# Performance work log

Measured on AMD Instinct MI355X. Metric: run time of the kernel, lower is better.

The kernel has to match this reference:

```python
import jax, jax.numpy as jnp
import numpy as np

EMBED_DIM = 1024
N_HEADS = 16

def setup_inputs() -> dict:
    key = jax.random.key(0)
    k1, k2, k3 = jax.random.split(key, 3)
    x = jax.random.normal(k1, (4, 2048, EMBED_DIM), dtype=jnp.float32)
    # nn.Linear(D, 3D): store weight as [D, 3D] for x @ W
    W_qkv = jax.random.normal(k2, (EMBED_DIM, 3 * EMBED_DIM), dtype=jnp.float32) * (1.0 / np.sqrt(EMBED_DIM))
    b_qkv = jax.random.normal(k3, (3 * EMBED_DIM,), dtype=jnp.float32) * 0.02
    return {"x": x, "W_qkv": W_qkv, "b_qkv": b_qkv}

def reference(x, W_qkv, b_qkv):
    bs, T, D = x.shape
    nh = N_HEADS
    hs = D // nh
    # fused qkv projection -> [bs, T, nh, 3, hs] (matches view(bs,T,nh,3*hs) + split(hs))
    qkv = (jnp.einsum('btd,de->bte', x, W_qkv) + b_qkv).reshape(bs, T, nh, 3, hs)
    q = qkv[..., 0, :].transpose(0, 2, 1, 3)  # [bs, nh, T, hs]
    k = qkv[..., 1, :].transpose(0, 2, 1, 3)
    v = qkv[..., 2, :].transpose(0, 2, 1, 3)
    scale = 1.0 / np.sqrt(hs).astype(np.float32)
    scores = jnp.einsum('bhqd,bhkd->bhqk', q, k) * scale  # [bs, nh, T, T]
    attn = jax.nn.softmax(scores, axis=-1)
    out = jnp.einsum('bhqk,bhkd->bhqd', attn, v)  # [bs, nh, T, hs]
    return out.transpose(0, 2, 1, 3).reshape(bs, T, D)
```

## Files before the change

kernel.cpp:

```cpp
#include <hip/hip_runtime.h>
#include <stdint.h>

#define T_SEQ 2048
#define DMODEL 1024
#define NHEAD 16
#define HS 64
#define N3 3072
#define BSZ 4
#define MTOT (BSZ*T_SEQ)

typedef __attribute__((ext_vector_type(8))) short bf16x8;
typedef __attribute__((ext_vector_type(4))) float f32x4;
typedef __attribute__((ext_vector_type(16))) float f32x16;
typedef __attribute__((ext_vector_type(2))) unsigned int uint2v;

#define QSCALE 0.18033688011112042f
#define SM_SHIFT 12.0f

#define BH_STRIDE 131072

__device__ inline unsigned short f2bf(float f){
  union { float f; uint32_t u; } v; v.f = f;
  uint32_t r = (v.u + 0x7fffu + ((v.u >> 16) & 1u)) >> 16;
  return (unsigned short)r;
}

__device__ inline uint32_t cvtpk_bf16(float lo, float hi){
  uint32_t r;
  asm("v_cvt_pk_bf16_f32 %0, %1, %2" : "=v"(r) : "v"(lo), "v"(hi));
  return r;
}

__device__ inline void plswap(uint32_t &a, uint32_t &b){
  uint2v r = __builtin_amdgcn_permlane32_swap(a, b, false, false);
  a = r[0]; b = r[1];
}

__device__ inline void gld16(const void* g, void* l){
  __builtin_amdgcn_global_load_lds((const __attribute__((address_space(1))) void*)g,
                                   (__attribute__((address_space(3))) void*)l, 16, 0, 0);
}

__global__ __launch_bounds__(256) void cvt_x(const float* __restrict__ x,
                                             unsigned short* __restrict__ xb, int n){
  int stride = gridDim.x * blockDim.x;
  for (int i = blockIdx.x * blockDim.x + threadIdx.x; i * 4 < n; i += stride){
    const float4 v = *(const float4*)(x + (size_t)i * 4);
    ushort4 o; o.x = f2bf(v.x); o.y = f2bf(v.y); o.z = f2bf(v.z); o.w = f2bf(v.w);
    *(ushort4*)(xb + (size_t)i * 4) = o;
  }
}

__global__ __launch_bounds__(256) void cvt_wt(const float* __restrict__ W,
                                              unsigned short* __restrict__ Wt){
  __shared__ float tile[32][33];
  int bx = blockIdx.x;
  int by = blockIdx.y;
  int tx = threadIdx.x;
  int ty = threadIdx.y;
#pragma unroll
  for (int i = 0; i < 4; i++){
    int k = by * 32 + ty + i * 8;
    int n = bx * 32 + tx;
    tile[ty + i * 8][tx] = W[(size_t)k * N3 + n];
  }
  __syncthreads();
#pragma unroll
  for (int i = 0; i < 4; i++){
    int n = bx * 32 + ty + i * 8;
    int k = by * 32 + tx;
    Wt[(size_t)n * DMODEL + k] = f2bf(tile[tx][ty + i * 8]);
  }
}

#define BM 128
#define BN 128
#define BK 32

__global__ __launch_bounds__(256, 2) void gemm_qkv(
    const unsigned short* __restrict__ xb, const unsigned short* __restrict__ wt,
    const float* __restrict__ bias,
    unsigned short* __restrict__ Qb, unsigned short* __restrict__ Kb,
    unsigned short* __restrict__ Vt)
{
  __shared__ unsigned short Al[2][BM * BK];
  __shared__ unsigned short Bl[2][BN * BK];
  const int tid = threadIdx.x;
  const int lane = tid & 63;
  const int w  = tid >> 6;
  const int wm = w >> 1, wn = w & 1;
  const int lr = lane & 15, lg = lane >> 4;
  const int m0 = blockIdx.x * BM;
  const int n0 = blockIdx.y * BN;

  f32x4 acc[4][4] = {};

  const int srow = tid >> 2;
  const int scol = ((tid & 3) ^ ((srow >> 1) & 3)) * 8;
  const unsigned short* ga0 = xb + (size_t)(m0 + srow) * DMODEL + scol;
  const unsigned short* gb0 = wt + (size_t)(n0 + srow) * DMODEL + scol;

  const int lgp = lg ^ ((lr >> 1) & 3);

  gld16(ga0,                         &Al[0][tid * 8]);
  gld16(ga0 + (size_t)64 * DMODEL,   &Al[0][tid * 8 + 2048]);
  gld16(gb0,                         &Bl[0][tid * 8]);
  gld16(gb0 + (size_t)64 * DMODEL,   &Bl[0][tid * 8 + 2048]);
  __syncthreads();

  for (int k0 = 0; k0 < DMODEL; k0 += BK){
    const int cur = (k0 >> 5) & 1;
    if (k0 + BK < DMODEL){
      gld16(ga0 + k0 + BK,                       &Al[cur ^ 1][tid * 8]);
      gld16(ga0 + k0 + BK + (size_t)64 * DMODEL, &Al[cur ^ 1][tid * 8 + 2048]);
      gld16(gb0 + k0 + BK,                       &Bl[cur ^ 1][tid * 8]);
      gld16(gb0 + k0 + BK + (size_t)64 * DMODEL, &Bl[cur ^ 1][tid * 8 + 2048]);
    }

    bf16x8 af[4], bfg[4];
#pragma unroll
    for (int i = 0; i < 4; i++){
      af[i]  = *(const bf16x8*)&Al[cur][(wm * 64 + i * 16 + lr) * BK + lgp * 8];
      bfg[i] = *(const bf16x8*)&Bl[cur][(wn * 64 + i * 16 + lr) * BK + lgp * 8];
    }
    __builtin_amdgcn_s_setprio(1);
#pragma unroll
    for (int i = 0; i < 4; i++)
#pragma unroll
      for (int j = 0; j < 4; j++)
        acc[i][j] = __builtin_amdgcn_mfma_f32_16x16x32_bf16(af[i], bfg[j], acc[i][j], 0, 0, 0);
    __builtin_amdgcn_s_setprio(0);

    __syncthreads();
  }

#pragma unroll
  for (int i = 0; i < 4; i++){
#pragma unroll
    for (int j = 0; j < 4; j++){
      int gn = n0 + wn * 64 + j * 16 + lr;
      float bv = bias[gn];
      int h = gn / 192;
      int rem = gn - h * 192;
      int which = rem >> 6;
      int d = rem & 63;
#pragma unroll
      for (int r = 0; r < 4; r++){
        int gm = m0 + wm * 64 + i * 16 + lg * 4 + r;
        int b = gm >> 11, t = gm & 2047;
        float val = acc[i][j][r] + bv;
        size_t base = (size_t)(b * NHEAD + h) * BH_STRIDE + (size_t)(t >> 5) * 2048;
        if (which == 0)
          Qb[base + (d >> 4) * 512 + ((d >> 3) & 1) * 256 + (t & 31) * 8 + (d & 7)] = f2bf(val * QSCALE);
        else if (which == 1)
          Kb[base + (d >> 4) * 512 + ((d >> 3) & 1) * 256 + (t & 31) * 8 + (d & 7)] = f2bf(val);
        else {
          int kv = t & 31;
          Vt[base + (d >> 5) * 1024 + (kv >> 4) * 512 + ((kv >> 3) & 1) * 256 + (d & 31) * 8 + (kv & 7)] = f2bf(val);
        }
      }
    }
  }
}

__global__ __launch_bounds__(256, 3) void attn(
    const unsigned short* __restrict__ Qb, const unsigned short* __restrict__ Kb,
    const unsigned short* __restrict__ Vt, float* __restrict__ out)
{
  __shared__ unsigned short KVs[2][2][2][2048];

  int flat = blockIdx.x + (blockIdx.y << 4) + (blockIdx.z << 8);
  int wid = (flat & 7) * 128 + (flat >> 3);
  const int bx = wid & 15;
  const int h  = (wid >> 4) & 15;
  const int b  = wid >> 8;

  const int tid = threadIdx.x;
  const int lane = tid & 63;
  const int w = tid >> 6;
  const int ql = lane & 31;
  const int hi = lane >> 5;
  const int bh = b * NHEAD + h;
  const int q0 = bx * 128 + w * 32;

  const unsigned short* Qf = Qb + (size_t)bh * BH_STRIDE;
  const unsigned short* Kg = Kb + (size_t)bh * BH_STRIDE;
  const unsigned short* Vg = Vt + (size_t)bh * BH_STRIDE;

  bf16x8 qf[4];
#pragma unroll
  for (int c = 0; c < 4; c++)
    qf[c] = *(const bf16x8*)(Qf + (size_t)(q0 >> 5) * 2048 + c * 512 + lane * 8);

  f32x16 cinit;
#pragma unroll
  for (int r = 0; r < 16; r++) cinit[r] = -SM_SHIFT;

  f32x16 acc0 = {}, acc1 = {};
  float lA = 0.f, lB = 0.f, lC = 0.f, lD = 0.f;

  gld16(Kg +        tid * 8, &KVs[0][0][0][tid * 8]);
  gld16(Kg + 2048 + tid * 8, &KVs[0][0][1][tid * 8]);
  gld16(Vg +        tid * 8, &KVs[0][1][0][tid * 8]);
  gld16(Vg + 2048 + tid * 8, &KVs[0][1][1][tid * 8]);
  __syncthreads();

#define SOFTMAX_PACK(S, PF1, PF2) \
    uint32_t c8[8]; \
    _Pragma("unroll") \
    for (int i = 0; i < 8; i += 2){ \
      float p0 = __builtin_amdgcn_exp2f((S)[2 * i]); \
      float p1 = __builtin_amdgcn_exp2f((S)[2 * i + 1]); \
      float p2 = __builtin_amdgcn_exp2f((S)[2 * i + 2]); \
      float p3 = __builtin_amdgcn_exp2f((S)[2 * i + 3]); \
      lA += p0; lB += p1; lC += p2; lD += p3; \
      c8[i]     = cvtpk_bf16(p0, p1); \
      c8[i + 1] = cvtpk_bf16(p2, p3); \
    } \
    plswap(c8[0], c8[2]); plswap(c8[1], c8[3]); \
    plswap(c8[4], c8[6]); plswap(c8[5], c8[7]); \
    PF1.u[0] = c8[0]; PF1.u[1] = c8[1]; PF1.u[2] = c8[2]; PF1.u[3] = c8[3]; \
    PF2.u[0] = c8[4]; PF2.u[1] = c8[5]; PF2.u[2] = c8[6]; PF2.u[3] = c8[7];

  for (int t = 0; t < 32; ++t){
    const int cur = t & 1;
    if (t < 31){
      const size_t g0 = (size_t)(2 * t + 2) * 2048 + tid * 8;
      gld16(Kg + g0,        &KVs[cur ^ 1][0][0][tid * 8]);
      gld16(Kg + g0 + 2048, &KVs[cur ^ 1][0][1][tid * 8]);
      gld16(Vg + g0,        &KVs[cur ^ 1][1][0][tid * 8]);
      gld16(Vg + g0 + 2048, &KVs[cur ^ 1][1][1][tid * 8]);
    }

    f32x16 sA;
    {
      bf16x8 kf[4];
#pragma unroll
      for (int c = 0; c < 4; c++) kf[c] = *(const bf16x8*)&KVs[cur][0][0][c * 512 + lane * 8];
      __builtin_amdgcn_s_setprio(1);
      sA = __builtin_amdgcn_mfma_f32_32x32x16_bf16(kf[0], qf[0], cinit, 0, 0, 0);
      sA = __builtin_amdgcn_mfma_f32_32x32x16_bf16(kf[1], qf[1], sA, 0, 0, 0);
      sA = __builtin_amdgcn_mfma_f32_32x32x16_bf16(kf[2], qf[2], sA, 0, 0, 0);
      sA = __builtin_amdgcn_mfma_f32_32x32x16_bf16(kf[3], qf[3], sA, 0, 0, 0);
      __builtin_amdgcn_s_setprio(0);
    }
    f32x16 sB;
    {
      bf16x8 kf[4];
#pragma unroll
      for (int c = 0; c < 4; c++) kf[c] = *(const bf16x8*)&KVs[cur][0][1][c * 512 + lane * 8];
      __builtin_amdgcn_s_setprio(1);
      sB = __builtin_amdgcn_mfma_f32_32x32x16_bf16(kf[0], qf[0], cinit, 0, 0, 0);
      sB = __builtin_amdgcn_mfma_f32_32x32x16_bf16(kf[1], qf[1], sB, 0, 0, 0);
      sB = __builtin_amdgcn_mfma_f32_32x32x16_bf16(kf[2], qf[2], sB, 0, 0, 0);
      sB = __builtin_amdgcn_mfma_f32_32x32x16_bf16(kf[3], qf[3], sB, 0, 0, 0);
      __builtin_amdgcn_s_setprio(0);
    }

    {
      union { uint32_t u[4]; bf16x8 v; } pf1, pf2;
      SOFTMAX_PACK(sA, pf1, pf2)
      bf16x8 vf[4];
#pragma unroll
      for (int c = 0; c < 4; c++) vf[c] = *(const bf16x8*)&KVs[cur][1][0][c * 512 + lane * 8];
      __builtin_amdgcn_s_setprio(1);
      acc0 = __builtin_amdgcn_mfma_f32_32x32x16_bf16(vf[0], pf1.v, acc0, 0, 0, 0);
      acc0 = __builtin_amdgcn_mfma_f32_32x32x16_bf16(vf[1], pf2.v, acc0, 0, 0, 0);
      acc1 = __builtin_amdgcn_mfma_f32_32x32x16_bf16(vf[2], pf1.v, acc1, 0, 0, 0);
      acc1 = __builtin_amdgcn_mfma_f32_32x32x16_bf16(vf[3], pf2.v, acc1, 0, 0, 0);
      __builtin_amdgcn_s_setprio(0);
    }
    {
      union { uint32_t u[4]; bf16x8 v; } pf1, pf2;
      SOFTMAX_PACK(sB, pf1, pf2)
      bf16x8 vf[4];
#pragma unroll
      for (int c = 0; c < 4; c++) vf[c] = *(const bf16x8*)&KVs[cur][1][1][c * 512 + lane * 8];
      __builtin_amdgcn_s_setprio(1);
      acc0 = __builtin_amdgcn_mfma_f32_32x32x16_bf16(vf[0], pf1.v, acc0, 0, 0, 0);
      acc0 = __builtin_amdgcn_mfma_f32_32x32x16_bf16(vf[1], pf2.v, acc0, 0, 0, 0);
      acc1 = __builtin_amdgcn_mfma_f32_32x32x16_bf16(vf[2], pf1.v, acc1, 0, 0, 0);
      acc1 = __builtin_amdgcn_mfma_f32_32x32x16_bf16(vf[3], pf2.v, acc1, 0, 0, 0);
      __builtin_amdgcn_s_setprio(0);
    }

    __syncthreads();
  }
#undef SOFTMAX_PACK

  float l_ = (lA + lB) + (lC + lD);
  l_ += __shfl_xor(l_, 32);
  float inv = 1.0f / l_;

  float* tl = (float*)&KVs[0][0][0][0];
  float* tw = tl + w * (32 * 33);
#pragma unroll
  for (int t2 = 0; t2 < 2; t2++){
    const f32x16& A = t2 ? acc1 : acc0;
#pragma unroll
    for (int r = 0; r < 16; r++){
      int dp = (r & 3) + 8 * (r >> 2) + 4 * hi;
      tw[dp * 33 + ql] = A[r] * inv;
    }
    asm volatile("s_waitcnt lgkmcnt(0)" ::: "memory");
    const int cq = lane >> 3;
    const int cc = (lane & 7) * 4;
#pragma unroll
    for (int it = 0; it < 4; it++){
      int q = it * 8 + cq;
      float4 o;
      o.x = tw[(cc + 0) * 33 + q];
      o.y = tw[(cc + 1) * 33 + q];
      o.z = tw[(cc + 2) * 33 + q];
      o.w = tw[(cc + 3) * 33 + q];
      *(float4*)(out + ((size_t)(b * T_SEQ + q0 + q)) * DMODEL + h * HS + t2 * 32 + cc) = o;
    }
    asm volatile("s_waitcnt lgkmcnt(0)" ::: "memory");
  }
}

extern "C" void kernel_launch(void* const* d_in, const int* in_sizes, int n_in,
                              void* d_out, int out_size, void* d_ws, size_t ws_size,
                              hipStream_t stream) {
  const float* x  = (const float*)d_in[0];
  const float* Wq = (const float*)d_in[1];
  const float* bq = (const float*)d_in[2];
  float* out = (float*)d_out;
  uint8_t* ws = (uint8_t*)d_ws;

  unsigned short* xb = (unsigned short*)(ws);
  unsigned short* wt = (unsigned short*)(ws + (size_t)16 * 1024 * 1024);
  unsigned short* Qb = (unsigned short*)(ws + (size_t)22 * 1024 * 1024);
  unsigned short* Kb = (unsigned short*)(ws + (size_t)38 * 1024 * 1024);
  unsigned short* Vt = (unsigned short*)(ws + (size_t)54 * 1024 * 1024);

  cvt_x<<<2048, 256, 0, stream>>>(x, xb, MTOT * DMODEL);
  cvt_wt<<<dim3(N3 / 32, DMODEL / 32), dim3(32, 8), 0, stream>>>(Wq, wt);
  gemm_qkv<<<dim3(MTOT / BM, N3 / BN), 256, 0, stream>>>(xb, wt, bq, Qb, Kb, Vt);
  attn<<<dim3(T_SEQ / 128, NHEAD, BSZ), 256, 0, stream>>>(Qb, Kb, Vt, out);
}
```

Baseline: 165.6 us.

## Triple-buffer QKV GEMM LDS loads with two-tile prefetch and explicit vmcnt waits

Converts the QKV projection GEMM from double to triple LDS buffering, keeping two K-tiles in flight. Each iteration issues the load two tiles ahead, waits with s_waitcnt vmcnt(8) for only the current tile, and uses raw barriers instead of __syncthreads. The aim is to hide global-load latency behind the MFMA work. In exchange LDS use grows by half, which may lower occupancy, and the tail iterations redundantly reload tile 31.

```diff
diff --git a/kernel.cpp b/kernel.cpp
--- a/kernel.cpp
+++ b/kernel.cpp
@@ -83,8 +83,8 @@
     unsigned short* __restrict__ Qb, unsigned short* __restrict__ Kb,
     unsigned short* __restrict__ Vt)
 {
-  __shared__ unsigned short Al[2][BM * BK];
-  __shared__ unsigned short Bl[2][BN * BK];
+  __shared__ unsigned short Al[3][BM * BK];
+  __shared__ unsigned short Bl[3][BN * BK];
   const int tid = threadIdx.x;
   const int lane = tid & 63;
   const int w  = tid >> 6;
@@ -102,20 +102,24 @@
 
   const int lgp = lg ^ ((lr >> 1) & 3);
 
-  gld16(ga0,                         &Al[0][tid * 8]);
-  gld16(ga0 + (size_t)64 * DMODEL,   &Al[0][tid * 8 + 2048]);
-  gld16(gb0,                         &Bl[0][tid * 8]);
-  gld16(gb0 + (size_t)64 * DMODEL,   &Bl[0][tid * 8 + 2048]);
-  __syncthreads();
-
-  for (int k0 = 0; k0 < DMODEL; k0 += BK){
-    const int cur = (k0 >> 5) & 1;
-    if (k0 + BK < DMODEL){
-      gld16(ga0 + k0 + BK,                       &Al[cur ^ 1][tid * 8]);
-      gld16(ga0 + k0 + BK + (size_t)64 * DMODEL, &Al[cur ^ 1][tid * 8 + 2048]);
-      gld16(gb0 + k0 + BK,                       &Bl[cur ^ 1][tid * 8]);
-      gld16(gb0 + k0 + BK + (size_t)64 * DMODEL, &Bl[cur ^ 1][tid * 8 + 2048]);
-    }
+#define STAGE(KT, B) { \
+    gld16(ga0 + (KT) * BK,                       &Al[B][tid * 8]); \
+    gld16(ga0 + (KT) * BK + (size_t)64 * DMODEL, &Al[B][tid * 8 + 2048]); \
+    gld16(gb0 + (KT) * BK,                       &Bl[B][tid * 8]); \
+    gld16(gb0 + (KT) * BK + (size_t)64 * DMODEL, &Bl[B][tid * 8 + 2048]); }
+
+  STAGE(0, 0)
+  STAGE(1, 1)
+
+  for (int kt = 0; kt < 32; ++kt){
+    const int cur = kt % 3;
+    const int nxt = (kt + 2) % 3;
+    __builtin_amdgcn_s_barrier();
+    const int ksrc = (kt + 2 <= 31) ? (kt + 2) : 31;
+    STAGE(ksrc, nxt)
+    asm volatile("s_waitcnt vmcnt(8)" ::: "memory");
+    __builtin_amdgcn_s_barrier();
+    __builtin_amdgcn_sched_barrier(0);
 
     bf16x8 af[4], bfg[4];
 #pragma unroll
@@ -130,9 +134,8 @@
       for (int j = 0; j < 4; j++)
         acc[i][j] = __builtin_amdgcn_mfma_f32_16x16x32_bf16(af[i], bfg[j], acc[i][j], 0, 0, 0);
     __builtin_amdgcn_s_setprio(0);
-
-    __syncthreads();
-  }
+  }
+#undef STAGE
 
 #pragma unroll
   for (int i = 0; i < 4; i++){
```

After: 168.6 us. About the same (+1.8%).
